# Kernel optimization log

Hardware: AMD Instinct MI355X
Metric: run time of the kernel (lower is better)

## Reference

```python
import jax, jax.numpy as jnp
import numpy as np
import math

N_HEADS = 8
EMBED = 128
HEAD_DEPTH = EMBED // N_HEADS
CLIP = 10.0
NEG_INF = 1.0e10
SCALE = math.sqrt(HEAD_DEPTH)


def setup_inputs() -> dict:
    key = jax.random.key(0)
    ks = jax.random.split(key, 8)
    B, C, N = 32, 2, 512
    Q = jax.random.normal(ks[0], (B, C, N, EMBED), dtype=jnp.float32)
    K = jax.random.normal(ks[1], (B, C, N, EMBED), dtype=jnp.float32)
    V = jax.random.normal(ks[2], (B, C, N, EMBED), dtype=jnp.float32)
    mask = jax.random.bernoulli(ks[3], 0.15, (B, C, N, 1))  # True = masked out
    stdv_qkv = 1.0 / math.sqrt(HEAD_DEPTH)
    stdv_out = 1.0 / math.sqrt(EMBED)
    # torch nn.Linear weights: (out_features, in_features)
    Wq = jax.random.uniform(ks[4], (EMBED, EMBED), jnp.float32, -stdv_qkv, stdv_qkv)
    Wk = jax.random.uniform(ks[5], (EMBED, EMBED), jnp.float32, -stdv_qkv, stdv_qkv)
    Wv = jax.random.uniform(ks[6], (EMBED, EMBED), jnp.float32, -stdv_qkv, stdv_qkv)
    Wout = jax.random.uniform(ks[7], (EMBED, EMBED), jnp.float32, -stdv_out, stdv_out)
    return {"Q": Q, "K": K, "V": V, "mask": mask,
            "Wq": Wq, "Wk": Wk, "Wv": Wv, "Wout": Wout}


def _split_heads(T):
    # (b, c, n, E) -> (b, H, c, n, d)
    b, c, n, _ = T.shape
    return T.reshape(b, c, n, N_HEADS, HEAD_DEPTH).transpose(0, 3, 1, 2, 4)


def reference(Q, K, V, mask, Wq, Wk, Wv, Wout):
    # Linear projections (torch Linear: y = x @ W.T)
    q = _split_heads(jnp.einsum('bcne,fe->bcnf', Q, Wq))
    k = _split_heads(jnp.einsum('bcne,fe->bcnf', K, Wk))
    v = _split_heads(jnp.einsum('bcne,fe->bcnf', V, Wv))
    # logits: (b, H, c, q, k)
    logits = jnp.einsum('bhcqd,bhckd->bhcqk', q, k) / SCALE
    logits = CLIP * jnp.tanh(logits)
    # mask (b, c, n, 1) -> (b, 1, c, 1, n); True -> -1e10
    m = mask[:, None, :, :, :].swapaxes(-1, -2)
    logits = jnp.where(m, -NEG_INF, logits)
    probs = jax.nn.softmax(logits, axis=-1)
    out = jnp.einsum('bhcqk,bhckd->bhcqd', probs, v)
    # combine heads: (b, H, c, n, d) -> (b, c, n, E)
    b, h, c, n, d = out.shape
    out = out.transpose(0, 2, 3, 1, 4).reshape(b, c, n, EMBED)
    return jnp.einsum('bcne,fe->bcnf', out, Wout)
```

## Files before the change

kernel.cpp:

```cpp
#include <hip/hip_runtime.h>

typedef _Float16 half_t;
typedef _Float16 half8 __attribute__((ext_vector_type(8)));
typedef _Float16 half4 __attribute__((ext_vector_type(4)));
typedef float floatx4 __attribute__((ext_vector_type(4)));
typedef float floatx16 __attribute__((ext_vector_type(16)));

#define C1 0.72134752044448170368f
#define C2 14.4269504088896340736f
#define C3 28.8539008177792681472f

__device__ __forceinline__ floatx4 zero4() {
    floatx4 z; z[0] = z[1] = z[2] = z[3] = 0.f; return z;
}
__device__ __forceinline__ floatx16 zero16() {
    floatx16 z;
#pragma unroll
    for (int i = 0; i < 16; ++i) z[i] = 0.f;
    return z;
}

__device__ __forceinline__ float pfun(float sp, float b) {
    float u = __builtin_amdgcn_exp2f(sp);
    float r = __builtin_amdgcn_rcpf(u + 1.0f);
    return __builtin_amdgcn_exp2f(b - C3 * r);
}

__global__ void k_convw(const float* __restrict__ Wq, const float* __restrict__ Wk,
                        const float* __restrict__ Wv, const float* __restrict__ Wo,
                        half_t* __restrict__ Wh) {
    int idx = blockIdx.x * 256 + threadIdx.x;
    int which = idx >> 14;
    int off = idx & 16383;
    const float* src = (which == 0) ? Wq : (which == 1) ? Wk : (which == 2) ? Wv : Wo;
    float scale = (which == 0) ? C1 : 1.0f;
    Wh[idx] = (half_t)(src[off] * scale);
}

__global__ __launch_bounds__(256) void k_proj(
        const float* __restrict__ Q, const float* __restrict__ K,
        const float* __restrict__ V, const half_t* __restrict__ WhBase,
        half_t* __restrict__ qw, half_t* __restrict__ kw, half_t* __restrict__ vw) {
    int which = blockIdx.y;
    const float* X = (which == 0) ? Q : (which == 1) ? K : V;
    const half_t* W = WhBase + which * 16384;

    int tid = threadIdx.x;
    int w = tid >> 6, lane = tid & 63;
    int l15 = lane & 15, quad = lane >> 4;
    int tokbase = blockIdx.x * 64 + w * 16;

    floatx4 acc[8];
#pragma unroll
    for (int nt = 0; nt < 8; ++nt) acc[nt] = zero4();

#pragma unroll
    for (int ks = 0; ks < 4; ++ks) {
        const float* ap = X + (tokbase + l15) * 128 + ks * 32 + quad * 8;
        float4 a0 = *(const float4*)ap;
        float4 a1 = *(const float4*)(ap + 4);
        half8 xf;
        xf[0] = (half_t)a0.x; xf[1] = (half_t)a0.y; xf[2] = (half_t)a0.z; xf[3] = (half_t)a0.w;
        xf[4] = (half_t)a1.x; xf[5] = (half_t)a1.y; xf[6] = (half_t)a1.z; xf[7] = (half_t)a1.w;
        if (which == 2) {
#pragma unroll
            for (int nt = 0; nt < 8; ++nt) {
                half8 wf = *(const half8*)(W + (nt * 16 + l15) * 128 + ks * 32 + quad * 8);
                acc[nt] = __builtin_amdgcn_mfma_f32_16x16x32_f16(xf, wf, acc[nt], 0, 0, 0);
            }
        } else {
#pragma unroll
            for (int nt = 0; nt < 8; ++nt) {
                half8 wf = *(const half8*)(W + (nt * 16 + l15) * 128 + ks * 32 + quad * 8);
                acc[nt] = __builtin_amdgcn_mfma_f32_16x16x32_f16(wf, xf, acc[nt], 0, 0, 0);
            }
        }
    }

    if (which == 2) {
        int R0 = tokbase + quad * 4;
        int bc = R0 >> 9, n0 = R0 & 511;
#pragma unroll
        for (int nt = 0; nt < 8; ++nt) {
            half4 hv;
            hv[0] = (half_t)acc[nt][0]; hv[1] = (half_t)acc[nt][1];
            hv[2] = (half_t)acc[nt][2]; hv[3] = (half_t)acc[nt][3];
            *(half4*)(vw + ((bc * 8 + nt) * 16 + l15) * 512 + n0) = hv;
        }
    } else {
        int R = tokbase + l15;
        int bc = R >> 9, n = R & 511;
        half_t* Y = (which == 0) ? qw : kw;
#pragma unroll
        for (int nt = 0; nt < 8; ++nt) {
            half4 hv;
            hv[0] = (half_t)acc[nt][0]; hv[1] = (half_t)acc[nt][1];
            hv[2] = (half_t)acc[nt][2]; hv[3] = (half_t)acc[nt][3];
            *(half4*)(Y + ((bc * 8 + nt) * 512 + n) * 16 + quad * 4) = hv;
        }
    }
}

__global__ __launch_bounds__(128, 8) void k_attn(
        const half_t* __restrict__ qg, const half_t* __restrict__ kg,
        const half_t* __restrict__ vTg, const int* __restrict__ mask,
        half_t* __restrict__ attn) {
    __shared__ float bias[512];
    __shared__ half_t Pl[2][32 * 36];

    int bx = blockIdx.x;
    int bch = bx >> 3, qe = bx & 7;
    int bc = bch >> 3, h = bch & 7;
    int tid = threadIdx.x;
    int w = tid >> 6, lane = tid & 63;
    int l31 = lane & 31, hf = lane >> 5;
    int l15 = lane & 15, quad = lane >> 4;

    const half_t* qh = qg + bch * 8192;
    const half_t* kh = kg + bch * 8192;
    const half_t* vh = vTg + bch * 8192;

#pragma unroll
    for (int i = 0; i < 4; ++i)
        bias[i * 128 + tid] = mask[bc * 512 + i * 128 + tid] ? -1.0e30f : C2;
    __syncthreads();

    int qbase = qe * 64 + w * 32;
    half8 qf = *(const half8*)(qh + (qbase + l31) * 16 + hf * 8);

    half8 ones;
#pragma unroll
    for (int j = 0; j < 8; ++j) ones[j] = (half_t)1.0f;

    floatx4 O[2], Os[2];
    O[0] = zero4(); O[1] = zero4();
    Os[0] = zero4(); Os[1] = zero4();
    half_t* Pw = &Pl[w][0];
    const float4* b4 = (const float4*)bias;

    half8 kf = *(const half8*)(kh + l31 * 16 + hf * 8);
    half8 vf = *(const half8*)(vh + l15 * 512 + quad * 8);

#pragma unroll 1
    for (int c = 0; c < 16; ++c) {
        half8 kf_n, vf_n;
        if (c < 15) {
            kf_n = *(const half8*)(kh + ((c + 1) * 32 + l31) * 16 + hf * 8);
            vf_n = *(const half8*)(vh + l15 * 512 + (c + 1) * 32 + quad * 8);
        }
        float4 bv[4];
#pragma unroll
        for (int g = 0; g < 4; ++g) bv[g] = b4[c * 8 + hf + 2 * g];

        floatx16 S = __builtin_amdgcn_mfma_f32_32x32x16_f16(kf, qf, zero16(), 0, 0, 0);
#pragma unroll
        for (int g = 0; g < 4; ++g) {
            float p0 = pfun(S[4 * g + 0], bv[g].x);
            float p1 = pfun(S[4 * g + 1], bv[g].y);
            float p2 = pfun(S[4 * g + 2], bv[g].z);
            float p3 = pfun(S[4 * g + 3], bv[g].w);
            auto t0 = __builtin_amdgcn_cvt_pkrtz(p0, p1);
            auto t1 = __builtin_amdgcn_cvt_pkrtz(p2, p3);
            half4 ph;
            ph[0] = (half_t)t0[0]; ph[1] = (half_t)t0[1];
            ph[2] = (half_t)t1[0]; ph[3] = (half_t)t1[1];
            *(half4*)(Pw + l31 * 36 + hf * 4 + g * 8) = ph;
        }
#pragma unroll
        for (int nt2 = 0; nt2 < 2; ++nt2) {
            half8 pb = *(const half8*)(Pw + (nt2 * 16 + l15) * 36 + quad * 8);
            O[nt2]  = __builtin_amdgcn_mfma_f32_16x16x32_f16(vf,   pb, O[nt2],  0, 0, 0);
            Os[nt2] = __builtin_amdgcn_mfma_f32_16x16x32_f16(ones, pb, Os[nt2], 0, 0, 0);
        }
        kf = kf_n; vf = vf_n;
    }

#pragma unroll
    for (int nt = 0; nt < 2; ++nt) {
        float iv = __builtin_amdgcn_rcpf(Os[nt][0]);
        int qrow = qbase + nt * 16 + l15;
        half4 ov;
        ov[0] = (half_t)(O[nt][0] * iv);
        ov[1] = (half_t)(O[nt][1] * iv);
        ov[2] = (half_t)(O[nt][2] * iv);
        ov[3] = (half_t)(O[nt][3] * iv);
        *(half4*)(attn + (bc * 512 + qrow) * 128 + h * 16 + quad * 4) = ov;
    }
}

__global__ __launch_bounds__(256) void k_out(
        const half_t* __restrict__ A, const half_t* __restrict__ Wh,
        float* __restrict__ out) {
    int tid = threadIdx.x;
    int w = tid >> 6, lane = tid & 63;
    int l15 = lane & 15, quad = lane >> 4;
    int tokbase = blockIdx.x * 64 + w * 16;

    floatx4 acc[8];
#pragma unroll
    for (int nt = 0; nt < 8; ++nt) acc[nt] = zero4();
#pragma unroll
    for (int ks = 0; ks < 4; ++ks) {
        half8 xf = *(const half8*)(A + (tokbase + l15) * 128 + ks * 32 + quad * 8);
#pragma unroll
        for (int nt = 0; nt < 8; ++nt) {
            half8 wf = *(const half8*)(Wh + (nt * 16 + l15) * 128 + ks * 32 + quad * 8);
            acc[nt] = __builtin_amdgcn_mfma_f32_16x16x32_f16(wf, xf, acc[nt], 0, 0, 0);
        }
    }
#pragma unroll
    for (int nt = 0; nt < 8; ++nt) {
        float4 o;
        o.x = acc[nt][0]; o.y = acc[nt][1]; o.z = acc[nt][2]; o.w = acc[nt][3];
        *(float4*)(out + (tokbase + l15) * 128 + nt * 16 + quad * 4) = o;
    }
}

extern "C" void kernel_launch(void* const* d_in, const int* in_sizes, int n_in,
                              void* d_out, int out_size, void* d_ws, size_t ws_size,
                              hipStream_t stream) {
    const float* Q    = (const float*)d_in[0];
    const float* K    = (const float*)d_in[1];
    const float* V    = (const float*)d_in[2];
    const int*   mask = (const int*)d_in[3];
    const float* Wq   = (const float*)d_in[4];
    const float* Wk   = (const float*)d_in[5];
    const float* Wv   = (const float*)d_in[6];
    const float* Wo   = (const float*)d_in[7];
    float* out = (float*)d_out;

    half_t* ws = (half_t*)d_ws;
    half_t* Wh = ws;
    half_t* qw = ws + 65536;
    half_t* kw = qw + 4194304;
    half_t* vw = kw + 4194304;
    half_t* aw = vw + 4194304;

    k_convw<<<256, 256, 0, stream>>>(Wq, Wk, Wv, Wo, Wh);
    k_proj<<<dim3(512, 3), 256, 0, stream>>>(Q, K, V, Wh, qw, kw, vw);
    k_attn<<<4096, 128, 0, stream>>>(qw, kw, vw, mask, aw);
    k_out<<<512, 256, 0, stream>>>(aw, Wh + 49152, out);
}
```

Measured before the change: 181.2 us.

## Software-pipeline attention loop so next chunk's QK and exp overlap PV MFMAs

Restructures the attention inner loop into a two-stage software pipeline. The QK^T MFMA and exp/softmax transform for chunk c+1 are issued while the PV and rowsum MFMAs for chunk c run, and K/V loads are prefetched two chunks ahead. The goal is to hide MFMA latency and the LDS round trip behind transcendental ALU work. To make room for the extra live registers, the occupancy hint drops from 8 to 6 waves per EU, so fewer waves are resident.

```diff
diff --git a/kernel.cpp b/kernel.cpp
--- a/kernel.cpp
+++ b/kernel.cpp
@@ -101,7 +101,7 @@
     }
 }
 
-__global__ __launch_bounds__(128, 8) void k_attn(
+__global__ __launch_bounds__(128, 6) void k_attn(
         const half_t* __restrict__ qg, const half_t* __restrict__ kg,
         const half_t* __restrict__ vTg, const int* __restrict__ mask,
         half_t* __restrict__ attn) {
@@ -138,41 +138,67 @@
     half_t* Pw = &Pl[w][0];
     const float4* b4 = (const float4*)bias;
 
-    half8 kf = *(const half8*)(kh + l31 * 16 + hf * 8);
-    half8 vf = *(const half8*)(vh + l15 * 512 + quad * 8);
+    half8 kf_nx = *(const half8*)(kh + (32 + l31) * 16 + hf * 8);
+    half8 vf_cur = *(const half8*)(vh + l15 * 512 + quad * 8);
+    half8 vf_nx  = *(const half8*)(vh + l15 * 512 + 32 + quad * 8);
+    half4 ph[4];
+    {
+        half8 kf0 = *(const half8*)(kh + l31 * 16 + hf * 8);
+        floatx16 S = __builtin_amdgcn_mfma_f32_32x32x16_f16(kf0, qf, zero16(), 0, 0, 0);
+#pragma unroll
+        for (int g = 0; g < 4; ++g) {
+            float4 bv = b4[hf + 2 * g];
+            float p0 = pfun(S[4 * g + 0], bv.x);
+            float p1 = pfun(S[4 * g + 1], bv.y);
+            float p2 = pfun(S[4 * g + 2], bv.z);
+            float p3 = pfun(S[4 * g + 3], bv.w);
+            auto t0 = __builtin_amdgcn_cvt_pkrtz(p0, p1);
+            auto t1 = __builtin_amdgcn_cvt_pkrtz(p2, p3);
+            ph[g][0] = (half_t)t0[0]; ph[g][1] = (half_t)t0[1];
+            ph[g][2] = (half_t)t1[0]; ph[g][3] = (half_t)t1[1];
+        }
+    }
 
 #pragma unroll 1
     for (int c = 0; c < 16; ++c) {
-        half8 kf_n, vf_n;
+#pragma unroll
+        for (int g = 0; g < 4; ++g)
+            *(half4*)(Pw + l31 * 36 + hf * 4 + g * 8) = ph[g];
+        half8 pb0 = *(const half8*)(Pw + l15 * 36 + quad * 8);
+        half8 pb1 = *(const half8*)(Pw + (16 + l15) * 36 + quad * 8);
+
         if (c < 15) {
-            kf_n = *(const half8*)(kh + ((c + 1) * 32 + l31) * 16 + hf * 8);
-            vf_n = *(const half8*)(vh + l15 * 512 + (c + 1) * 32 + quad * 8);
-        }
-        float4 bv[4];
-#pragma unroll
-        for (int g = 0; g < 4; ++g) bv[g] = b4[c * 8 + hf + 2 * g];
-
-        floatx16 S = __builtin_amdgcn_mfma_f32_32x32x16_f16(kf, qf, zero16(), 0, 0, 0);
-#pragma unroll
-        for (int g = 0; g < 4; ++g) {
-            float p0 = pfun(S[4 * g + 0], bv[g].x);
-            float p1 = pfun(S[4 * g + 1], bv[g].y);
-            float p2 = pfun(S[4 * g + 2], bv[g].z);
-            float p3 = pfun(S[4 * g + 3], bv[g].w);
-            auto t0 = __builtin_amdgcn_cvt_pkrtz(p0, p1);
-            auto t1 = __builtin_amdgcn_cvt_pkrtz(p2, p3);
-            half4 ph;
-            ph[0] = (half_t)t0[0]; ph[1] = (half_t)t0[1];
-            ph[2] = (half_t)t1[0]; ph[3] = (half_t)t1[1];
-            *(half4*)(Pw + l31 * 36 + hf * 4 + g * 8) = ph;
-        }
-#pragma unroll
-        for (int nt2 = 0; nt2 < 2; ++nt2) {
-            half8 pb = *(const half8*)(Pw + (nt2 * 16 + l15) * 36 + quad * 8);
-            O[nt2]  = __builtin_amdgcn_mfma_f32_16x16x32_f16(vf,   pb, O[nt2],  0, 0, 0);
-            Os[nt2] = __builtin_amdgcn_mfma_f32_16x16x32_f16(ones, pb, Os[nt2], 0, 0, 0);
-        }
-        kf = kf_n; vf = vf_n;
+            floatx16 S = __builtin_amdgcn_mfma_f32_32x32x16_f16(kf_nx, qf, zero16(), 0, 0, 0);
+            if (c < 14) {
+                kf_nx = *(const half8*)(kh + ((c + 2) * 32 + l31) * 16 + hf * 8);
+            }
+            half8 vf_n2;
+            if (c < 14) {
+                vf_n2 = *(const half8*)(vh + l15 * 512 + (c + 2) * 32 + quad * 8);
+            }
+#pragma unroll
+            for (int g = 0; g < 4; ++g) {
+                float4 bv = b4[(c + 1) * 8 + hf + 2 * g];
+                float p0 = pfun(S[4 * g + 0], bv.x);
+                float p1 = pfun(S[4 * g + 1], bv.y);
+                float p2 = pfun(S[4 * g + 2], bv.z);
+                float p3 = pfun(S[4 * g + 3], bv.w);
+                auto t0 = __builtin_amdgcn_cvt_pkrtz(p0, p1);
+                auto t1 = __builtin_amdgcn_cvt_pkrtz(p2, p3);
+                ph[g][0] = (half_t)t0[0]; ph[g][1] = (half_t)t0[1];
+                ph[g][2] = (half_t)t1[0]; ph[g][3] = (half_t)t1[1];
+            }
+            O[0]  = __builtin_amdgcn_mfma_f32_16x16x32_f16(vf_cur, pb0, O[0],  0, 0, 0);
+            Os[0] = __builtin_amdgcn_mfma_f32_16x16x32_f16(ones,   pb0, Os[0], 0, 0, 0);
+            O[1]  = __builtin_amdgcn_mfma_f32_16x16x32_f16(vf_cur, pb1, O[1],  0, 0, 0);
+            Os[1] = __builtin_amdgcn_mfma_f32_16x16x32_f16(ones,   pb1, Os[1], 0, 0, 0);
+            vf_cur = vf_nx; vf_nx = vf_n2;
+        } else {
+            O[0]  = __builtin_amdgcn_mfma_f32_16x16x32_f16(vf_cur, pb0, O[0],  0, 0, 0);
+            Os[0] = __builtin_amdgcn_mfma_f32_16x16x32_f16(ones,   pb0, Os[0], 0, 0, 0);
+            O[1]  = __builtin_amdgcn_mfma_f32_16x16x32_f16(vf_cur, pb1, O[1],  0, 0, 0);
+            Os[1] = __builtin_amdgcn_mfma_f32_16x16x32_f16(ones,   pb1, Os[1], 0, 0, 0);
+        }
     }
 
 #pragma unroll
```

Result: slower. 202.5 us (+11.8%).
